# Performance work log

Hardware: AMD Instinct MI355X
Metric: run time of the kernel (lower is better)

Reference implementation:

```python
import jax, jax.numpy as jnp
import numpy as np

U_N = 100000
I_N = 50000
EMB_DIM = 64
L_N = 3          # number of propagation layers
NNZ = 4_800_000  # edges in the normalized bipartite graph (avg degree ~32)


def setup_inputs() -> dict:
    key = jax.random.key(0)
    k_u, k_i, k_r, k_c, k_v = jax.random.split(key, 5)
    N = U_N + I_N
    # Xavier-uniform-ish embedding init
    lim = float(np.sqrt(6.0 / (U_N + EMB_DIM)))
    user_emb = jax.random.uniform(k_u, (U_N, EMB_DIM), jnp.float32, -lim, lim)
    lim_i = float(np.sqrt(6.0 / (I_N + EMB_DIM)))
    item_emb = jax.random.uniform(k_i, (I_N, EMB_DIM), jnp.float32, -lim_i, lim_i)
    # COO sparse graph over all N = u_n + i_n nodes
    row = jax.random.randint(k_r, (NNZ,), 0, N, jnp.int32)
    col = jax.random.randint(k_c, (NNZ,), 0, N, jnp.int32)
    # emulate symmetric-normalized adjacency values ~ 1/deg so propagation stays bounded
    vals = jax.random.uniform(k_v, (NNZ,), jnp.float32) * (1.0 / 32.0)
    return {"user_emb": user_emb, "item_emb": item_emb, "row": row, "col": col, "vals": vals}


def reference(user_emb, item_emb, row, col, vals):
    N = user_emb.shape[0] + item_emb.shape[0]
    all_emb = jnp.concatenate([user_emb, item_emb], axis=0)  # [N, D]
    emb0 = all_emb
    acc = all_emb  # running sum over layer embeddings (layer 0 included)
    x = all_emb
    for _ in range(L_N):
        # SpMM: out[r] += vals[e] * x[col[e]] for each edge e with row[e] == r
        x = jax.ops.segment_sum(vals[:, None] * x[col], row, num_segments=N)
        acc = acc + x
    out = acc / (L_N + 1)  # mean over stacked layer embeddings
    return (emb0, out)
```

## Files before the change

kernel.cpp:

```cpp
#include <hip/hip_runtime.h>

#define U_N 100000
#define I_N 50000
#define N_NODES 150000
#define EMB_D 64
#define NNZ 4800000
#define ND (N_NODES * EMB_D)
#define ND4 (ND / 4)
#define UD4 (U_N * EMB_D / 4)

#define RPB 1024
#define NB ((N_NODES + RPB - 1) / RPB)
#define TILE 4096
#define NTILE ((NNZ + TILE - 1) / TILE)

__device__ __forceinline__ unsigned short f2bf(float f) {
    unsigned int u = __float_as_uint(f);
    unsigned int r = (u + 0x7FFFu + ((u >> 16) & 1u)) >> 16;
    return (unsigned short)r;
}
__device__ __forceinline__ float bf2f(unsigned short h) {
    return __uint_as_float((unsigned int)h << 16);
}

__global__ void k_init(const float4* __restrict__ u, const float4* __restrict__ it,
                       float4* __restrict__ emb0, ushort4* __restrict__ hb0) {
    int i = blockIdx.x * blockDim.x + threadIdx.x;
    if (i >= ND4) return;
    float4 v = (i < UD4) ? u[i] : it[i - UD4];
    emb0[i] = v;
    ushort4 h;
    h.x = f2bf(v.x); h.y = f2bf(v.y); h.z = f2bf(v.z); h.w = f2bf(v.w);
    hb0[i] = h;
}

__global__ void k_bucket_hist(const int* __restrict__ row, int* __restrict__ bhist) {
    __shared__ int lh[NB];
    int t = threadIdx.x;
    for (int i = t; i < NB; i += 256) lh[i] = 0;
    __syncthreads();
    int base = blockIdx.x * TILE;
    int cnt = min(TILE, NNZ - base);
    for (int i = t; i < cnt; i += 256)
        atomicAdd(&lh[row[base + i] >> 10], 1);
    __syncthreads();
    for (int i = t; i < NB; i += 256)
        if (lh[i]) atomicAdd(&bhist[i], lh[i]);
}

__global__ void k_bucket_scan(const int* __restrict__ bhist, int* __restrict__ bbase,
                              int* __restrict__ bcur) {
    __shared__ int wsum[4];
    int t = threadIdx.x, lane = t & 63, wv = t >> 6;
    int v = (t < NB) ? bhist[t] : 0;
    int iv = v;
    for (int off = 1; off < 64; off <<= 1) {
        int u = __shfl_up(iv, off);
        if (lane >= off) iv += u;
    }
    if (lane == 63) wsum[wv] = iv;
    __syncthreads();
    int woff = 0;
    for (int w = 0; w < wv; ++w) woff += wsum[w];
    int ex = woff + iv - v;
    if (t < NB) { bbase[t] = ex; bcur[t] = ex; }
    if (t == NB - 1) bbase[NB] = ex + v;
}

__global__ void k_partition(const int* __restrict__ row, const int* __restrict__ col,
                            const float* __restrict__ vals, int* __restrict__ bcur,
                            int2* __restrict__ tmp) {
    __shared__ int2 stage[TILE];
    __shared__ unsigned char stageB[TILE];
    __shared__ int hist[NB];
    __shared__ int scn[NB];
    __shared__ int gbase[NB];
    __shared__ int wsum[4];
    int t = threadIdx.x;
    int lane = t & 63, wv = t >> 6;
    for (int i = t; i < NB; i += 256) hist[i] = 0;
    __syncthreads();
    int base = blockIdx.x * TILE;
    int cnt = min(TILE, NNZ - base);

    int  myb[16];
    int  myslot[16];
    int2 myp[16];
#pragma unroll
    for (int j = 0; j < 16; ++j) {
        int i = t + j * 256;
        myb[j] = -1;
        if (i < cnt) {
            int e = base + i;
            int r = row[e];
            int b = r >> 10;
            myb[j] = b;
            myp[j] = make_int2(((r & (RPB - 1)) << 18) | col[e], __float_as_int(vals[e]));
            myslot[j] = atomicAdd(&hist[b], 1);
        }
    }
    __syncthreads();
    int v = (t < NB) ? hist[t] : 0;
    int iv = v;
    for (int off = 1; off < 64; off <<= 1) {
        int u = __shfl_up(iv, off);
        if (lane >= off) iv += u;
    }
    if (lane == 63) wsum[wv] = iv;
    __syncthreads();
    int woff = 0;
    for (int w = 0; w < wv; ++w) woff += wsum[w];
    if (t < NB) scn[t] = woff + iv - v;
    if (t < NB && v > 0) gbase[t] = atomicAdd(&bcur[t], v);
    __syncthreads();
#pragma unroll
    for (int j = 0; j < 16; ++j) {
        if (myb[j] >= 0) {
            int pos = scn[myb[j]] + myslot[j];
            stage[pos] = myp[j];
            stageB[pos] = (unsigned char)myb[j];
        }
    }
    __syncthreads();
    for (int i = t; i < cnt; i += 256) {
        int b = stageB[i];
        tmp[gbase[b] + (i - scn[b])] = stage[i];
    }
}

__global__ void k_bucket_csr(const int* __restrict__ bbase, const int2* __restrict__ tmp,
                             int2* __restrict__ edges, int* __restrict__ rp) {
    __shared__ int lh[RPB];
    __shared__ int lsc[RPB];
    int b = blockIdx.x, t = threadIdx.x;
    int s0 = bbase[b], s1 = bbase[b + 1];
    int n = s1 - s0;
    lh[t] = 0;
    __syncthreads();
    for (int i = t; i < n; i += 1024)
        atomicAdd(&lh[(unsigned)tmp[s0 + i].x >> 18], 1);
    __syncthreads();
    int v = lh[t];
    lsc[t] = v;
    __syncthreads();
    for (int off = 1; off < 1024; off <<= 1) {
        int add = (t >= off) ? lsc[t - off] : 0;
        __syncthreads();
        lsc[t] += add;
        __syncthreads();
    }
    int excl = lsc[t] - v;
    int r = b * RPB + t;
    if (r < N_NODES) rp[r] = s0 + excl;
    if (b == NB - 1 && t == 0) rp[N_NODES] = NNZ;
    __syncthreads();
    lh[t] = excl;
    __syncthreads();
    for (int i = t; i < n; i += 1024) {
        int2 p = tmp[s0 + i];
        int rl = (unsigned)p.x >> 18;
        int pos = s0 + atomicAdd(&lh[rl], 1);
        edges[pos] = make_int2(p.x & 0x3FFFF, p.y);
    }
}

__device__ __forceinline__ float row_dot(const int* __restrict__ rp,
                                         const int2* __restrict__ edges,
                                         const unsigned short* __restrict__ x,
                                         int wid, int lane) {
    int start = __builtin_amdgcn_readfirstlane(rp[wid]);
    int end   = __builtin_amdgcn_readfirstlane(rp[wid + 1]);
    float s0 = 0.f, s1 = 0.f, s2 = 0.f, s3 = 0.f;
    int e = start;
    for (; e + 16 <= end; e += 16) {
        int2 E[16];
#pragma unroll
        for (int j = 0; j < 16; ++j) E[j] = edges[e + j];
        float g[16];
#pragma unroll
        for (int j = 0; j < 16; ++j) g[j] = bf2f(x[(size_t)E[j].x * EMB_D + lane]);
#pragma unroll
        for (int j = 0; j < 16; ++j) {
            float p = __int_as_float(E[j].y) * g[j];
            if ((j & 3) == 0) s0 += p;
            else if ((j & 3) == 1) s1 += p;
            else if ((j & 3) == 2) s2 += p;
            else s3 += p;
        }
    }
    int rem = end - e;
    if (rem > 0) {
        int2 E[16];
#pragma unroll
        for (int j = 0; j < 16; ++j) E[j] = edges[e + j];
#pragma unroll
        for (int j = 0; j < 16; ++j)
            if (j >= rem) { E[j].x = 0; E[j].y = 0; }
        float g[16];
#pragma unroll
        for (int j = 0; j < 16; ++j) g[j] = bf2f(x[(size_t)E[j].x * EMB_D + lane]);
#pragma unroll
        for (int j = 0; j < 16; ++j) {
            float p = __int_as_float(E[j].y) * g[j];
            if ((j & 3) == 0) s0 += p;
            else if ((j & 3) == 1) s1 += p;
            else if ((j & 3) == 2) s2 += p;
            else s3 += p;
        }
    }
    return (s0 + s1) + (s2 + s3);
}

__global__ void k_spmm_mid(const int* __restrict__ rp, const int2* __restrict__ edges,
                           const unsigned short* __restrict__ x,
                           unsigned short* __restrict__ y) {
    int wid = blockIdx.x * (blockDim.x >> 6) + (threadIdx.x >> 6);
    if (wid >= N_NODES) return;
    int lane = threadIdx.x & 63;
    float s = row_dot(rp, edges, x, wid, lane);
    y[(size_t)wid * EMB_D + lane] = f2bf(s);
}

__global__ void k_spmm_fin(const int* __restrict__ rp, const int2* __restrict__ edges,
                           const unsigned short* __restrict__ x,
                           const float* __restrict__ emb0,
                           const unsigned short* __restrict__ y1,
                           const unsigned short* __restrict__ y2,
                           float* __restrict__ acc) {
    int wid = blockIdx.x * (blockDim.x >> 6) + (threadIdx.x >> 6);
    if (wid >= N_NODES) return;
    int lane = threadIdx.x & 63;
    float s = row_dot(rp, edges, x, wid, lane);
    size_t o = (size_t)wid * EMB_D + lane;
    acc[o] = (emb0[o] + bf2f(y1[o]) + bf2f(y2[o]) + s) * 0.25f;
}

extern "C" void kernel_launch(void* const* d_in, const int* in_sizes, int n_in,
                              void* d_out, int out_size, void* d_ws, size_t ws_size,
                              hipStream_t stream) {
    const float* user_emb = (const float*)d_in[0];
    const float* item_emb = (const float*)d_in[1];
    const int*   row      = (const int*)d_in[2];
    const int*   col      = (const int*)d_in[3];
    const float* vals     = (const float*)d_in[4];

    float* emb0 = (float*)d_out;
    float* acc  = (float*)d_out + ND;

    int2* tmp   = (int2*)d_ws;
    int2* edges = tmp + NNZ;
    unsigned short* hb2 = (unsigned short*)(edges + NNZ);
    int*  ibase = (int*)(hb2 + ND);
    int*  rp    = ibase;
    int*  bhist = ibase + N_NODES + 1;
    int*  bbase = bhist + NB;
    int*  bcur  = bbase + NB + 1;
    unsigned short* hb0 = (unsigned short*)d_ws;
    unsigned short* hb1 = hb0 + ND;

    const int BLK = 256;
    const int grid_nd = (ND4 + BLK - 1) / BLK;
    const int grid_spmm = (N_NODES * 64 + BLK - 1) / BLK;

    hipMemsetAsync(bhist, 0, NB * sizeof(int), stream);
    k_bucket_hist<<<NTILE, BLK, 0, stream>>>(row, bhist);
    k_bucket_scan<<<1, 256, 0, stream>>>(bhist, bbase, bcur);
    k_partition<<<NTILE, BLK, 0, stream>>>(row, col, vals, bcur, tmp);
    k_bucket_csr<<<NB, 1024, 0, stream>>>(bbase, tmp, edges, rp);

    k_init<<<grid_nd, BLK, 0, stream>>>((const float4*)user_emb,
                                        (const float4*)item_emb,
                                        (float4*)emb0, (ushort4*)hb0);

    k_spmm_mid<<<grid_spmm, BLK, 0, stream>>>(rp, edges, hb0, hb1);
    k_spmm_mid<<<grid_spmm, BLK, 0, stream>>>(rp, edges, hb1, hb2);
    k_spmm_fin<<<grid_spmm, BLK, 0, stream>>>(rp, edges, hb2, emb0, hb1, hb2, acc);
}
```

Before: 583.9 us.

## Replace two-pass bucket partition CSR build with global-atomic counting sort

The CSR build now does a per-row count with global atomics, a hierarchical scan, and a direct atomic scatter of edges into row slots. This replaces the bucket histogram, partition, and per-bucket sort kernels. The fp32-to-bf16 init is fused into the histogram kernel. The change drops the intermediate tmp buffer and one full pass over the edges, at the cost of heavy contended global atomics and random scattered writes. Edge order within a row becomes nondeterministic, so summation order can vary between runs.

New measurement: 979.3 us. +67.7%, slower.

```diff
diff --git a/kernel.cpp b/kernel.cpp
--- a/kernel.cpp
+++ b/kernel.cpp
@@ -9,10 +9,12 @@
 #define ND4 (ND / 4)
 #define UD4 (U_N * EMB_D / 4)
 
-#define RPB 1024
-#define NB ((N_NODES + RPB - 1) / RPB)
-#define TILE 4096
-#define NTILE ((NNZ + TILE - 1) / TILE)
+#define SCB 1024
+#define NSB ((N_NODES + SCB - 1) / SCB)
+#define NQ4 (NNZ / 4)
+
+#define GRID_INIT ((ND4 + 255) / 256)
+#define GRID_EDGE ((NQ4 + 255) / 256)
 
 __device__ __forceinline__ unsigned short f2bf(float f) {
     unsigned int u = __float_as_uint(f);
@@ -23,36 +25,45 @@
     return __uint_as_float((unsigned int)h << 16);
 }
 
-__global__ void k_init(const float4* __restrict__ u, const float4* __restrict__ it,
-                       float4* __restrict__ emb0, ushort4* __restrict__ hb0) {
-    int i = blockIdx.x * blockDim.x + threadIdx.x;
-    if (i >= ND4) return;
-    float4 v = (i < UD4) ? u[i] : it[i - UD4];
-    emb0[i] = v;
-    ushort4 h;
-    h.x = f2bf(v.x); h.y = f2bf(v.y); h.z = f2bf(v.z); h.w = f2bf(v.w);
-    hb0[i] = h;
-}
-
-__global__ void k_bucket_hist(const int* __restrict__ row, int* __restrict__ bhist) {
-    __shared__ int lh[NB];
-    int t = threadIdx.x;
-    for (int i = t; i < NB; i += 256) lh[i] = 0;
+__global__ void k_init_hist(const float4* __restrict__ u, const float4* __restrict__ it,
+                            float4* __restrict__ emb0, ushort4* __restrict__ hb0,
+                            const int4* __restrict__ row4, int* __restrict__ rcount) {
+    int b = blockIdx.x;
+    if (b < GRID_INIT) {
+        int i = b * 256 + threadIdx.x;
+        if (i >= ND4) return;
+        float4 v = (i < UD4) ? u[i] : it[i - UD4];
+        emb0[i] = v;
+        ushort4 h;
+        h.x = f2bf(v.x); h.y = f2bf(v.y); h.z = f2bf(v.z); h.w = f2bf(v.w);
+        hb0[i] = h;
+    } else {
+        int i = (b - GRID_INIT) * 256 + threadIdx.x;
+        if (i >= NQ4) return;
+        int4 r = row4[i];
+        atomicAdd(&rcount[r.x], 1);
+        atomicAdd(&rcount[r.y], 1);
+        atomicAdd(&rcount[r.z], 1);
+        atomicAdd(&rcount[r.w], 1);
+    }
+}
+
+__global__ void k_block_sums(const int4* __restrict__ rcount4, int* __restrict__ bsum) {
+    __shared__ int wsum[4];
+    int b = blockIdx.x, t = threadIdx.x;
+    int lane = t & 63, wv = t >> 6;
+    int4 r = rcount4[b * 256 + t];
+    int s = r.x + r.y + r.z + r.w;
+    for (int off = 32; off > 0; off >>= 1) s += __shfl_down(s, off);
+    if (lane == 0) wsum[wv] = s;
     __syncthreads();
-    int base = blockIdx.x * TILE;
-    int cnt = min(TILE, NNZ - base);
-    for (int i = t; i < cnt; i += 256)
-        atomicAdd(&lh[row[base + i] >> 10], 1);
-    __syncthreads();
-    for (int i = t; i < NB; i += 256)
-        if (lh[i]) atomicAdd(&bhist[i], lh[i]);
-}
-
-__global__ void k_bucket_scan(const int* __restrict__ bhist, int* __restrict__ bbase,
-                              int* __restrict__ bcur) {
+    if (t == 0) bsum[b] = wsum[0] + wsum[1] + wsum[2] + wsum[3];
+}
+
+__global__ void k_scan_bsum(const int* __restrict__ bsum, int* __restrict__ bbase) {
     __shared__ int wsum[4];
     int t = threadIdx.x, lane = t & 63, wv = t >> 6;
-    int v = (t < NB) ? bhist[t] : 0;
+    int v = (t < NSB) ? bsum[t] : 0;
     int iv = v;
     for (int off = 1; off < 64; off <<= 1) {
         int u = __shfl_up(iv, off);
@@ -62,45 +73,16 @@
     __syncthreads();
     int woff = 0;
     for (int w = 0; w < wv; ++w) woff += wsum[w];
-    int ex = woff + iv - v;
-    if (t < NB) { bbase[t] = ex; bcur[t] = ex; }
-    if (t == NB - 1) bbase[NB] = ex + v;
-}
-
-__global__ void k_partition(const int* __restrict__ row, const int* __restrict__ col,
-                            const float* __restrict__ vals, int* __restrict__ bcur,
-                            int2* __restrict__ tmp) {
-    __shared__ int2 stage[TILE];
-    __shared__ unsigned char stageB[TILE];
-    __shared__ int hist[NB];
-    __shared__ int scn[NB];
-    __shared__ int gbase[NB];
-    __shared__ int wsum[4];
-    int t = threadIdx.x;
+    if (t < NSB) bbase[t] = woff + iv - v;
+}
+
+__global__ void k_scan_rows(const int* __restrict__ rcount, const int* __restrict__ bbase,
+                            int* __restrict__ rp, int* __restrict__ cur) {
+    __shared__ int wsum[16];
+    int b = blockIdx.x, t = threadIdx.x;
     int lane = t & 63, wv = t >> 6;
-    for (int i = t; i < NB; i += 256) hist[i] = 0;
-    __syncthreads();
-    int base = blockIdx.x * TILE;
-    int cnt = min(TILE, NNZ - base);
-
-    int  myb[16];
-    int  myslot[16];
-    int2 myp[16];
-#pragma unroll
-    for (int j = 0; j < 16; ++j) {
-        int i = t + j * 256;
-        myb[j] = -1;
-        if (i < cnt) {
-            int e = base + i;
-            int r = row[e];
-            int b = r >> 10;
-            myb[j] = b;
-            myp[j] = make_int2(((r & (RPB - 1)) << 18) | col[e], __float_as_int(vals[e]));
-            myslot[j] = atomicAdd(&hist[b], 1);
-        }
-    }
-    __syncthreads();
-    int v = (t < NB) ? hist[t] : 0;
+    int gid = b * SCB + t;
+    int v = rcount[gid];
     int iv = v;
     for (int off = 1; off < 64; off <<= 1) {
         int u = __shfl_up(iv, off);
@@ -110,58 +92,26 @@
     __syncthreads();
     int woff = 0;
     for (int w = 0; w < wv; ++w) woff += wsum[w];
-    if (t < NB) scn[t] = woff + iv - v;
-    if (t < NB && v > 0) gbase[t] = atomicAdd(&bcur[t], v);
-    __syncthreads();
-#pragma unroll
-    for (int j = 0; j < 16; ++j) {
-        if (myb[j] >= 0) {
-            int pos = scn[myb[j]] + myslot[j];
-            stage[pos] = myp[j];
-            stageB[pos] = (unsigned char)myb[j];
-        }
-    }
-    __syncthreads();
-    for (int i = t; i < cnt; i += 256) {
-        int b = stageB[i];
-        tmp[gbase[b] + (i - scn[b])] = stage[i];
-    }
-}
-
-__global__ void k_bucket_csr(const int* __restrict__ bbase, const int2* __restrict__ tmp,
-                             int2* __restrict__ edges, int* __restrict__ rp) {
-    __shared__ int lh[RPB];
-    __shared__ int lsc[RPB];
-    int b = blockIdx.x, t = threadIdx.x;
-    int s0 = bbase[b], s1 = bbase[b + 1];
-    int n = s1 - s0;
-    lh[t] = 0;
-    __syncthreads();
-    for (int i = t; i < n; i += 1024)
-        atomicAdd(&lh[(unsigned)tmp[s0 + i].x >> 18], 1);
-    __syncthreads();
-    int v = lh[t];
-    lsc[t] = v;
-    __syncthreads();
-    for (int off = 1; off < 1024; off <<= 1) {
-        int add = (t >= off) ? lsc[t - off] : 0;
-        __syncthreads();
-        lsc[t] += add;
-        __syncthreads();
-    }
-    int excl = lsc[t] - v;
-    int r = b * RPB + t;
-    if (r < N_NODES) rp[r] = s0 + excl;
-    if (b == NB - 1 && t == 0) rp[N_NODES] = NNZ;
-    __syncthreads();
-    lh[t] = excl;
-    __syncthreads();
-    for (int i = t; i < n; i += 1024) {
-        int2 p = tmp[s0 + i];
-        int rl = (unsigned)p.x >> 18;
-        int pos = s0 + atomicAdd(&lh[rl], 1);
-        edges[pos] = make_int2(p.x & 0x3FFFF, p.y);
-    }
+    int ex = bbase[b] + woff + iv - v;
+    if (gid <= N_NODES) rp[gid] = ex;
+    if (gid < N_NODES) cur[gid] = ex;
+}
+
+__global__ void k_scatter(const int4* __restrict__ row4, const int4* __restrict__ col4,
+                          const float4* __restrict__ val4, int* __restrict__ cur,
+                          int2* __restrict__ edges) {
+    int i = blockIdx.x * blockDim.x + threadIdx.x;
+    if (i >= NQ4) return;
+    int4 r = row4[i], c = col4[i];
+    float4 v = val4[i];
+    int p0 = atomicAdd(&cur[r.x], 1);
+    int p1 = atomicAdd(&cur[r.y], 1);
+    int p2 = atomicAdd(&cur[r.z], 1);
+    int p3 = atomicAdd(&cur[r.w], 1);
+    edges[p0] = make_int2(c.x, __float_as_int(v.x));
+    edges[p1] = make_int2(c.y, __float_as_int(v.y));
+    edges[p2] = make_int2(c.z, __float_as_int(v.z));
+    edges[p3] = make_int2(c.w, __float_as_int(v.w));
 }
 
 __device__ __forceinline__ float row_dot(const int* __restrict__ rp,
@@ -247,30 +197,28 @@
     float* emb0 = (float*)d_out;
     float* acc  = (float*)d_out + ND;
 
-    int2* tmp   = (int2*)d_ws;
-    int2* edges = tmp + NNZ;
-    unsigned short* hb2 = (unsigned short*)(edges + NNZ);
-    int*  ibase = (int*)(hb2 + ND);
-    int*  rp    = ibase;
-    int*  bhist = ibase + N_NODES + 1;
-    int*  bbase = bhist + NB;
-    int*  bcur  = bbase + NB + 1;
-    unsigned short* hb0 = (unsigned short*)d_ws;
+    int2* edges = (int2*)d_ws;
+    unsigned short* hb0 = (unsigned short*)(edges + NNZ);
     unsigned short* hb1 = hb0 + ND;
+    unsigned short* hb2 = hb1 + ND;
+    int* rcount = (int*)(hb2 + ND);
+    int* rp     = rcount + NSB * SCB;
+    int* cur    = rp + N_NODES + 1;
+    int* bsum   = cur + N_NODES;
+    int* bbase  = bsum + NSB;
 
     const int BLK = 256;
-    const int grid_nd = (ND4 + BLK - 1) / BLK;
     const int grid_spmm = (N_NODES * 64 + BLK - 1) / BLK;
 
-    hipMemsetAsync(bhist, 0, NB * sizeof(int), stream);
-    k_bucket_hist<<<NTILE, BLK, 0, stream>>>(row, bhist);
-    k_bucket_scan<<<1, 256, 0, stream>>>(bhist, bbase, bcur);
-    k_partition<<<NTILE, BLK, 0, stream>>>(row, col, vals, bcur, tmp);
-    k_bucket_csr<<<NB, 1024, 0, stream>>>(bbase, tmp, edges, rp);
-
-    k_init<<<grid_nd, BLK, 0, stream>>>((const float4*)user_emb,
-                                        (const float4*)item_emb,
-                                        (float4*)emb0, (ushort4*)hb0);
+    hipMemsetAsync(rcount, 0, NSB * SCB * sizeof(int), stream);
+    k_init_hist<<<GRID_INIT + GRID_EDGE, BLK, 0, stream>>>(
+        (const float4*)user_emb, (const float4*)item_emb,
+        (float4*)emb0, (ushort4*)hb0, (const int4*)row, rcount);
+    k_block_sums<<<NSB, BLK, 0, stream>>>((const int4*)rcount, bsum);
+    k_scan_bsum<<<1, BLK, 0, stream>>>(bsum, bbase);
+    k_scan_rows<<<NSB, SCB, 0, stream>>>(rcount, bbase, rp, cur);
+    k_scatter<<<GRID_EDGE, BLK, 0, stream>>>((const int4*)row, (const int4*)col,
+                                             (const float4*)vals, cur, edges);
 
     k_spmm_mid<<<grid_spmm, BLK, 0, stream>>>(rp, edges, hb0, hb1);
     k_spmm_mid<<<grid_spmm, BLK, 0, stream>>>(rp, edges, hb1, hb2);
```

## Build CSR via global per-row histogram and atomic placement instead of bucket sort

Applied to the files above, without the earlier changes.

Replaces the coarse bucket histogram and per-bucket local CSR build with a global per-row count (global atomics), a two-level scan producing row pointers directly, and a placement kernel that scatters partitioned edges into final positions using per-row atomic cursors. The aim is to drop the serial 1024-wide shared-memory scan and low-parallelism per-bucket kernel (one block per 1024 rows) in favour of wide, fully parallel kernels. It adds more global atomic traffic and more kernel launches. The edge order within a row becomes nondeterministic, which can slightly change float summation order.

Result: slower. 884.2 us (+51.4%).

```diff
diff --git a/kernel.cpp b/kernel.cpp
--- a/kernel.cpp
+++ b/kernel.cpp
@@ -13,6 +13,10 @@
 #define NB ((N_NODES + RPB - 1) / RPB)
 #define TILE 4096
 #define NTILE ((NNZ + TILE - 1) / TILE)
+
+#define SCB 1024
+#define NSB ((N_NODES + SCB - 1) / SCB)
+#define NQ4 (NNZ / 4)
 
 __device__ __forceinline__ unsigned short f2bf(float f) {
     unsigned int u = __float_as_uint(f);
@@ -34,25 +38,32 @@
     hb0[i] = h;
 }
 
-__global__ void k_bucket_hist(const int* __restrict__ row, int* __restrict__ bhist) {
-    __shared__ int lh[NB];
-    int t = threadIdx.x;
-    for (int i = t; i < NB; i += 256) lh[i] = 0;
-    __syncthreads();
-    int base = blockIdx.x * TILE;
-    int cnt = min(TILE, NNZ - base);
-    for (int i = t; i < cnt; i += 256)
-        atomicAdd(&lh[row[base + i] >> 10], 1);
-    __syncthreads();
-    for (int i = t; i < NB; i += 256)
-        if (lh[i]) atomicAdd(&bhist[i], lh[i]);
-}
-
-__global__ void k_bucket_scan(const int* __restrict__ bhist, int* __restrict__ bbase,
-                              int* __restrict__ bcur) {
+__global__ void k_row_hist(const int4* __restrict__ row4, int* __restrict__ rcount) {
+    int i = blockIdx.x * blockDim.x + threadIdx.x;
+    if (i >= NQ4) return;
+    int4 r = row4[i];
+    atomicAdd(&rcount[r.x], 1);
+    atomicAdd(&rcount[r.y], 1);
+    atomicAdd(&rcount[r.z], 1);
+    atomicAdd(&rcount[r.w], 1);
+}
+
+__global__ void k_block_sums(const int4* __restrict__ rcount4, int* __restrict__ bsum) {
+    __shared__ int wsum[4];
+    int b = blockIdx.x, t = threadIdx.x;
+    int lane = t & 63, wv = t >> 6;
+    int4 r = rcount4[b * 256 + t];
+    int s = r.x + r.y + r.z + r.w;
+    for (int off = 32; off > 0; off >>= 1) s += __shfl_down(s, off);
+    if (lane == 0) wsum[wv] = s;
+    __syncthreads();
+    if (t == 0) bsum[b] = wsum[0] + wsum[1] + wsum[2] + wsum[3];
+}
+
+__global__ void k_scan_bsum(const int* __restrict__ bsum, int* __restrict__ bbase) {
     __shared__ int wsum[4];
     int t = threadIdx.x, lane = t & 63, wv = t >> 6;
-    int v = (t < NB) ? bhist[t] : 0;
+    int v = (t < NSB) ? bsum[t] : 0;
     int iv = v;
     for (int off = 1; off < 64; off <<= 1) {
         int u = __shfl_up(iv, off);
@@ -62,9 +73,30 @@
     __syncthreads();
     int woff = 0;
     for (int w = 0; w < wv; ++w) woff += wsum[w];
-    int ex = woff + iv - v;
-    if (t < NB) { bbase[t] = ex; bcur[t] = ex; }
-    if (t == NB - 1) bbase[NB] = ex + v;
+    if (t < NSB) bbase[t] = woff + iv - v;
+}
+
+__global__ void k_scan_rows(const int* __restrict__ rcount, const int* __restrict__ bbase,
+                            int* __restrict__ rp, int* __restrict__ cur,
+                            int* __restrict__ bcur) {
+    __shared__ int wsum[16];
+    int b = blockIdx.x, t = threadIdx.x;
+    int lane = t & 63, wv = t >> 6;
+    int gid = b * SCB + t;
+    int v = rcount[gid];
+    int iv = v;
+    for (int off = 1; off < 64; off <<= 1) {
+        int u = __shfl_up(iv, off);
+        if (lane >= off) iv += u;
+    }
+    if (lane == 63) wsum[wv] = iv;
+    __syncthreads();
+    int woff = 0;
+    for (int w = 0; w < wv; ++w) woff += wsum[w];
+    int ex = bbase[b] + woff + iv - v;
+    if (gid <= N_NODES) rp[gid] = ex;
+    if (gid < N_NODES) cur[gid] = ex;
+    if (t == 0) bcur[b] = ex;
 }
 
 __global__ void k_partition(const int* __restrict__ row, const int* __restrict__ col,
@@ -128,39 +160,44 @@
     }
 }
 
-__global__ void k_bucket_csr(const int* __restrict__ bbase, const int2* __restrict__ tmp,
-                             int2* __restrict__ edges, int* __restrict__ rp) {
-    __shared__ int lh[RPB];
-    __shared__ int lsc[RPB];
-    int b = blockIdx.x, t = threadIdx.x;
-    int s0 = bbase[b], s1 = bbase[b + 1];
-    int n = s1 - s0;
-    lh[t] = 0;
-    __syncthreads();
-    for (int i = t; i < n; i += 1024)
-        atomicAdd(&lh[(unsigned)tmp[s0 + i].x >> 18], 1);
-    __syncthreads();
-    int v = lh[t];
-    lsc[t] = v;
-    __syncthreads();
-    for (int off = 1; off < 1024; off <<= 1) {
-        int add = (t >= off) ? lsc[t - off] : 0;
-        __syncthreads();
-        lsc[t] += add;
-        __syncthreads();
-    }
-    int excl = lsc[t] - v;
-    int r = b * RPB + t;
-    if (r < N_NODES) rp[r] = s0 + excl;
-    if (b == NB - 1 && t == 0) rp[N_NODES] = NNZ;
-    __syncthreads();
-    lh[t] = excl;
-    __syncthreads();
-    for (int i = t; i < n; i += 1024) {
-        int2 p = tmp[s0 + i];
-        int rl = (unsigned)p.x >> 18;
-        int pos = s0 + atomicAdd(&lh[rl], 1);
-        edges[pos] = make_int2(p.x & 0x3FFFF, p.y);
+__global__ void k_place(const int* __restrict__ rp, const int2* __restrict__ tmp,
+                        int* __restrict__ cur, int2* __restrict__ edges) {
+    __shared__ int bb[NB + 1];
+    int t = threadIdx.x;
+    for (int j = t; j <= NB; j += 256) bb[j] = rp[min(j * RPB, N_NODES)];
+    __syncthreads();
+    int base = blockIdx.x * TILE;
+    int cnt = min(TILE, NNZ - base);
+    if (t >= cnt) return;
+    int2 E[16];
+#pragma unroll
+    for (int j = 0; j < 16; ++j) {
+        int i = t + j * 256;
+        if (i < cnt) E[j] = tmp[base + i];
+    }
+    int g0 = base + t;
+    int lo = 0, hi = NB - 1;
+    while (lo < hi) {
+        int mid = (lo + hi) >> 1;
+        if (bb[mid + 1] <= g0) lo = mid + 1; else hi = mid;
+    }
+    int b = lo;
+    int pos[16];
+#pragma unroll
+    for (int j = 0; j < 16; ++j) {
+        int i = t + j * 256;
+        if (i < cnt) {
+            int g = base + i;
+            while (g >= bb[b + 1]) ++b;
+            int r = (b << 10) + ((unsigned)E[j].x >> 18);
+            pos[j] = atomicAdd(&cur[r], 1);
+        }
+    }
+#pragma unroll
+    for (int j = 0; j < 16; ++j) {
+        int i = t + j * 256;
+        if (i < cnt)
+            edges[pos[j]] = make_int2(E[j].x & 0x3FFFF, E[j].y);
     }
 }
 
@@ -250,23 +287,28 @@
     int2* tmp   = (int2*)d_ws;
     int2* edges = tmp + NNZ;
     unsigned short* hb2 = (unsigned short*)(edges + NNZ);
-    int*  ibase = (int*)(hb2 + ND);
-    int*  rp    = ibase;
-    int*  bhist = ibase + N_NODES + 1;
-    int*  bbase = bhist + NB;
-    int*  bcur  = bbase + NB + 1;
+    int* rcount = (int*)(hb2 + ND);
+    int* rp     = rcount + NSB * SCB;
+    int* cur    = rp + N_NODES + 1;
+    int* bcur   = cur + N_NODES;
+    int* bsum   = bcur + NB;
+    int* bbase  = bsum + NSB;
     unsigned short* hb0 = (unsigned short*)d_ws;
     unsigned short* hb1 = hb0 + ND;
 
     const int BLK = 256;
     const int grid_nd = (ND4 + BLK - 1) / BLK;
+    const int grid_q4 = (NQ4 + BLK - 1) / BLK;
     const int grid_spmm = (N_NODES * 64 + BLK - 1) / BLK;
 
-    hipMemsetAsync(bhist, 0, NB * sizeof(int), stream);
-    k_bucket_hist<<<NTILE, BLK, 0, stream>>>(row, bhist);
-    k_bucket_scan<<<1, 256, 0, stream>>>(bhist, bbase, bcur);
+    hipMemsetAsync(rcount, 0, NSB * SCB * sizeof(int), stream);
+    k_row_hist<<<grid_q4, BLK, 0, stream>>>((const int4*)row, rcount);
+    k_block_sums<<<NSB, BLK, 0, stream>>>((const int4*)rcount, bsum);
+    k_scan_bsum<<<1, BLK, 0, stream>>>(bsum, bbase);
+    k_scan_rows<<<NSB, SCB, 0, stream>>>(rcount, bbase, rp, cur, bcur);
+
     k_partition<<<NTILE, BLK, 0, stream>>>(row, col, vals, bcur, tmp);
-    k_bucket_csr<<<NB, 1024, 0, stream>>>(bbase, tmp, edges, rp);
+    k_place<<<NTILE, BLK, 0, stream>>>(rp, tmp, cur, edges);
 
     k_init<<<grid_nd, BLK, 0, stream>>>((const float4*)user_emb,
                                         (const float4*)item_emb,
```
